# Optimization experiments

Hardware: AMD Instinct MI355X
Metric: run time of the kernel (lower is better)

## Reference

```python
import jax, jax.numpy as jnp
import numpy as np

MARGIN = 1.0


def setup_inputs() -> dict:
    key = jax.random.key(0)
    k1, k2, k3 = jax.random.split(key, 3)
    B, D, C = 16384, 256, 2000
    pred_embedding = jax.random.normal(k1, (B, D), dtype=jnp.float32)
    batch_label = jax.random.randint(k2, (B,), 0, C, dtype=jnp.int64)
    train_classes = jnp.arange(C, dtype=jnp.int64)
    train_sig = jax.random.normal(k3, (D, C), dtype=jnp.float32)
    return {
        "pred_embedding": pred_embedding,
        "batch_label": batch_label,
        "train_classes": train_classes,
        "train_sig": train_sig,
    }


def reference(pred_embedding, batch_label, train_classes, train_sig):
    # scores[j, k] = <pred_embedding[j], train_sig[:, train_classes[k]]>
    # Single GEMM replaces the per-pair dot-product loops.
    sig_cols = train_sig[:, train_classes]            # [D, C]
    scores = jnp.einsum("bd,dc->bc", pred_embedding, sig_cols)  # [B, C]
    # ground-truth class score per row: <XW_j, train_sig[:, y_j]>
    gt = jnp.einsum("bd,db->b", pred_embedding, train_sig[:, batch_label])  # [B]
    # exclude the class equal to the row label
    mask = (train_classes[None, :] != batch_label[:, None])  # [B, C] bool
    hinge = jnp.maximum(MARGIN + scores - gt[:, None], 0.0)
    loss = jnp.sum(jnp.where(mask, hinge, 0.0))
    return loss
```

## Files before the change

kernel.cpp:

```cpp
#include <hip/hip_runtime.h>

#define B_SZ 16384
#define D_SZ 256
#define C_SZ 2000
#define C_PAD 2048
#define MARGIN_F 1.0f
#define NBLK 1024

typedef float floatx16 __attribute__((ext_vector_type(16)));

__device__ inline void gld_lds16(const void* g, void* l) {
  __builtin_amdgcn_global_load_lds(
      (const __attribute__((address_space(1))) void*)g,
      (__attribute__((address_space(3))) void*)l, 16, 0, 0);
}


__device__ inline int2 pack8_fp8(const float* v) {
  int lo = __builtin_amdgcn_cvt_pk_fp8_f32(v[0], v[1], 0, false);
  lo = __builtin_amdgcn_cvt_pk_fp8_f32(v[2], v[3], lo, true);
  int hi = __builtin_amdgcn_cvt_pk_fp8_f32(v[4], v[5], 0, false);
  hi = __builtin_amdgcn_cvt_pk_fp8_f32(v[6], v[7], hi, true);
  return make_int2(lo, hi);
}
__device__ inline float rt_fp8(float x) {
  int p = __builtin_amdgcn_cvt_pk_fp8_f32(x, x, 0, false);
  return __builtin_amdgcn_cvt_f32_fp8(p, 0);
}

__global__ __launch_bounds__(256) void prep_kernel(
    const float* __restrict__ pred, const float* __restrict__ sig,
    const int* __restrict__ label, char* __restrict__ predq,
    char* __restrict__ sigq, float* __restrict__ gt) {
  int bid = (int)blockIdx.x;
  int tid = threadIdx.x;
  if (bid < 512) {
    __shared__ float ldsP[32][260];
#pragma unroll
    for (int it = 0; it < 8; it++) {
      int idx = it * 1024 + tid * 4;
      int r = idx >> 8, c = idx & 255;
      *(float4*)&ldsP[r][c] = *(const float4*)(pred + (size_t)(bid * 32 + r) * D_SZ + c);
    }
    __syncthreads();
#pragma unroll
    for (int it = 0; it < 4; it++) {
      int ch = it * 256 + tid;
      int lane = ch & 63, ks = ch >> 6;
      int r = lane & 31, kb = ks * 16 + (lane >> 5) * 8;
      float v[8];
#pragma unroll
      for (int j = 0; j < 8; j++) v[j] = ldsP[r][kb + j];
      *(int2*)(predq + ((size_t)(bid * 16 + ks) * 64 + lane) * 8) = pack8_fp8(v);
    }
    int lane = tid & 63, w = tid >> 6;
    for (int rr = 0; rr < 8; rr++) {
      int r = w * 8 + rr;
      int row = bid * 32 + r;
      int lbl = label[row];
      float s = 0.f;
#pragma unroll
      for (int i = 0; i < 4; i++)
        s += rt_fp8(ldsP[r][lane * 4 + i]) *
             rt_fp8(sig[(size_t)(lane * 4 + i) * C_SZ + lbl]);
#pragma unroll
      for (int off = 32; off > 0; off >>= 1) s += __shfl_down(s, off, 64);
      if (lane == 0) gt[row] = s;
    }
  } else {
    int ct = bid - 512;
#pragma unroll
    for (int it = 0; it < 4; it++) {
      int ch = it * 256 + tid;
      int lane = ch & 63, ks = ch >> 6;
      int col = ct * 32 + (lane & 31);
      int kb = ks * 16 + (lane >> 5) * 8;
      float v[8];
#pragma unroll
      for (int j = 0; j < 8; j++)
        v[j] = (col < C_SZ) ? sig[(size_t)(kb + j) * C_SZ + col] : 0.f;
      *(int2*)(sigq + ((size_t)(ct * 16 + ks) * 64 + lane) * 8) = pack8_fp8(v);
    }
  }
}

__global__ __launch_bounds__(256) void mfma_fused_kernel(
    const char* __restrict__ predq, const char* __restrict__ sigq,
    const float* __restrict__ gt, float* __restrict__ partial) {
  __shared__ char Bs[4096 * 8];
  __shared__ float red[4];
  int tid = threadIdx.x;
  int lane = tid & 63;
  int w = tid >> 6;
  int kh = lane >> 5, lm = lane & 31;
  int bid = (int)blockIdx.x;
  int i = bid >> 3;
  int rsb = (bid & 7) * 8 + (i & 7);
  int cg = i >> 3;

#pragma unroll
  for (int s = 0; s < 8; s++) {
    int q0 = s * 256 + w * 64;
    gld_lds16(sigq + ((size_t)cg * 2048 + q0 + lane) * 16, (void*)(Bs + (size_t)q0 * 16));
  }

  long afr[2][16];
#pragma unroll
  for (int rt = 0; rt < 2; rt++)
#pragma unroll
    for (int ks = 0; ks < 16; ks++)
      afr[rt][ks] = *(const long*)(predq +
          (((size_t)(rsb * 8 + w * 2 + rt) * 16 + ks) * 64 + lane) * 8);

  float mgv[2][16];
#pragma unroll
  for (int rt = 0; rt < 2; rt++)
#pragma unroll
    for (int reg = 0; reg < 16; reg++) {
      int row = rsb * 256 + w * 64 + rt * 32 + (reg & 3) + 8 * (reg >> 2) + 4 * kh;
      mgv[rt][reg] = MARGIN_F - gt[row];
    }
  __syncthreads();

  float sum = 0.f;
#pragma unroll
  for (int ct = 0; ct < 4; ct++) {
    floatx16 acc0 = {}, acc1 = {};
#pragma unroll
    for (int ks = 0; ks < 16; ks++) {
      long b = *(const long*)(Bs + (size_t)((ct * 16 + ks) * 64 + lane) * 8);
      acc0 = __builtin_amdgcn_mfma_f32_32x32x16_fp8_fp8(afr[0][ks], b, acc0, 0, 0, 0);
      acc1 = __builtin_amdgcn_mfma_f32_32x32x16_fp8_fp8(afr[1][ks], b, acc1, 0, 0, 0);
    }
    int col = cg * 128 + ct * 32 + lm;
    float keep = (col < C_SZ) ? 1.f : 0.f;
#pragma unroll
    for (int reg = 0; reg < 16; reg++) {
      sum += keep * fmaxf(acc0[reg] + mgv[0][reg], 0.f);
      sum += keep * fmaxf(acc1[reg] + mgv[1][reg], 0.f);
    }
  }
#pragma unroll
  for (int off = 32; off > 0; off >>= 1) sum += __shfl_down(sum, off, 64);
  if (lane == 0) red[w] = sum;
  __syncthreads();
  if (tid == 0) partial[bid] = red[0] + red[1] + red[2] + red[3];
}

__global__ __launch_bounds__(256) void reduce_kernel(
    const float* __restrict__ partial, float* __restrict__ out) {
  int tid = threadIdx.x;
  float s = 0.f;
  for (int i = tid * 4; i < NBLK; i += 1024) {
    float4 p = *(const float4*)(partial + i);
    s += p.x + p.y + p.z + p.w;
  }
#pragma unroll
  for (int off = 32; off > 0; off >>= 1) s += __shfl_down(s, off, 64);
  __shared__ float red[4];
  if ((tid & 63) == 0) red[tid >> 6] = s;
  __syncthreads();
  if (tid == 0) out[0] = red[0] + red[1] + red[2] + red[3] - (float)B_SZ * MARGIN_F;
}

extern "C" void kernel_launch(void* const* d_in, const int* in_sizes, int n_in,
                              void* d_out, int out_size, void* d_ws, size_t ws_size,
                              hipStream_t stream) {
  const float* pred  = (const float*)d_in[0];
  const int*   label = (const int*)d_in[1];
  const float* sig   = (const float*)d_in[3];
  float* out = (float*)d_out;

  float* gt      = (float*)d_ws;
  float* partial = (float*)((char*)d_ws + (64 << 10));
  char*  predq   = (char*)d_ws + (128 << 10);
  char*  sigq    = (char*)d_ws + (128 << 10) + (4 << 20);

  prep_kernel<<<576, 256, 0, stream>>>(pred, sig, label, predq, sigq, gt);
  mfma_fused_kernel<<<NBLK, 256, 0, stream>>>(predq, sigq, gt, partial);
  reduce_kernel<<<1, 256, 0, stream>>>(partial, out);
}
```

Measured before the change: 104.4 us.

## Fuse prep, GEMM-hinge and reduction into one cooperative kernel with grid syncs

Merges the three kernel launches into a single cooperative kernel of 1024 blocks. Two grid-wide barriers separate the quantization, MFMA hinge and final reduction phases, and the old three-launch path is kept as a fallback if the cooperative launch fails. The sig quantization work is spread over 256 blocks instead of 64. The goal is to remove launch gaps and tail idle time between the stages, at the cost of grid-sync overhead and a shared-memory/register budget capped to fit 4 blocks per CU so all blocks are co-resident.

```diff
diff --git a/kernel.cpp b/kernel.cpp
--- a/kernel.cpp
+++ b/kernel.cpp
@@ -1,4 +1,7 @@
 #include <hip/hip_runtime.h>
+#include <hip/hip_cooperative_groups.h>
+
+namespace cg = cooperative_groups;
 
 #define B_SZ 16384
 #define D_SZ 256
@@ -26,6 +29,126 @@
 __device__ inline float rt_fp8(float x) {
   int p = __builtin_amdgcn_cvt_pk_fp8_f32(x, x, 0, false);
   return __builtin_amdgcn_cvt_f32_fp8(p, 0);
+}
+
+__global__ __launch_bounds__(256, 4) void fused_all_kernel(
+    const float* __restrict__ pred, const float* __restrict__ sig,
+    const int* __restrict__ label, char* __restrict__ predq,
+    char* __restrict__ sigq, float* __restrict__ gt,
+    float* __restrict__ partial, float* __restrict__ out) {
+  __shared__ float ldsP[32][260];
+  __shared__ float gtS[256];
+  __shared__ float red[4];
+  char* Bs = (char*)&ldsP[0][0];
+
+  int bid = (int)blockIdx.x;
+  int tid = threadIdx.x;
+  int lane = tid & 63;
+  int w = tid >> 6;
+
+  if (bid < 512) {
+#pragma unroll
+    for (int it = 0; it < 8; it++) {
+      int idx = it * 1024 + tid * 4;
+      int r = idx >> 8, c = idx & 255;
+      *(float4*)&ldsP[r][c] = *(const float4*)(pred + (size_t)(bid * 32 + r) * D_SZ + c);
+    }
+    __syncthreads();
+#pragma unroll
+    for (int it = 0; it < 4; it++) {
+      int ch = it * 256 + tid;
+      int ln = ch & 63, ks = ch >> 6;
+      int r = ln & 31, kb = ks * 16 + (ln >> 5) * 8;
+      float v[8];
+#pragma unroll
+      for (int j = 0; j < 8; j++) v[j] = ldsP[r][kb + j];
+      *(int2*)(predq + ((size_t)(bid * 16 + ks) * 64 + ln) * 8) = pack8_fp8(v);
+    }
+    for (int rr = 0; rr < 8; rr++) {
+      int r = w * 8 + rr;
+      int row = bid * 32 + r;
+      int lbl = label[row];
+      float s = 0.f;
+#pragma unroll
+      for (int i = 0; i < 4; i++)
+        s += rt_fp8(ldsP[r][lane * 4 + i]) *
+             rt_fp8(sig[(size_t)(lane * 4 + i) * C_SZ + lbl]);
+#pragma unroll
+      for (int off = 32; off > 0; off >>= 1) s += __shfl_down(s, off, 64);
+      if (lane == 0) gt[row] = s;
+    }
+    __syncthreads();
+  } else if (bid < 768) {
+    int ch = (bid - 512) * 256 + tid;
+    int ln = ch & 63, ks = (ch >> 6) & 15, ct = ch >> 10;
+    int col = ct * 32 + (ln & 31);
+    int kb = ks * 16 + (ln >> 5) * 8;
+    float v[8];
+#pragma unroll
+    for (int j = 0; j < 8; j++)
+      v[j] = (col < C_SZ) ? sig[(size_t)(kb + j) * C_SZ + col] : 0.f;
+    *(int2*)(sigq + ((size_t)(ct * 16 + ks) * 64 + ln) * 8) = pack8_fp8(v);
+  }
+
+  cg::this_grid().sync();
+
+  int kh = lane >> 5, lm = lane & 31;
+  int i = bid >> 3;
+  int rsb = (bid & 7) * 8 + (i & 7);
+  int cg_ = i >> 3;
+
+#pragma unroll
+  for (int s = 0; s < 8; s++) {
+    int q0 = s * 256 + w * 64;
+    gld_lds16(sigq + ((size_t)cg_ * 2048 + q0 + lane) * 16, (void*)(Bs + (size_t)q0 * 16));
+  }
+  gtS[tid] = gt[rsb * 256 + tid];
+
+  long afr[2][16];
+#pragma unroll
+  for (int rt = 0; rt < 2; rt++)
+#pragma unroll
+    for (int ks = 0; ks < 16; ks++)
+      afr[rt][ks] = *(const long*)(predq +
+          (((size_t)(rsb * 8 + w * 2 + rt) * 16 + ks) * 64 + lane) * 8);
+  __syncthreads();
+
+  float sum = 0.f;
+#pragma unroll
+  for (int ct = 0; ct < 4; ct++) {
+    floatx16 acc0 = {}, acc1 = {};
+#pragma unroll
+    for (int ks = 0; ks < 16; ks++) {
+      long b = *(const long*)(Bs + (size_t)((ct * 16 + ks) * 64 + lane) * 8);
+      acc0 = __builtin_amdgcn_mfma_f32_32x32x16_fp8_fp8(afr[0][ks], b, acc0, 0, 0, 0);
+      acc1 = __builtin_amdgcn_mfma_f32_32x32x16_fp8_fp8(afr[1][ks], b, acc1, 0, 0, 0);
+    }
+    int col = cg_ * 128 + ct * 32 + lm;
+    float keep = (col < C_SZ) ? 1.f : 0.f;
+#pragma unroll
+    for (int reg = 0; reg < 16; reg++) {
+      int rl = (reg & 3) + 8 * (reg >> 2) + 4 * kh;
+      sum += keep * fmaxf(acc0[reg] + MARGIN_F - gtS[w * 64 + rl], 0.f);
+      sum += keep * fmaxf(acc1[reg] + MARGIN_F - gtS[w * 64 + 32 + rl], 0.f);
+    }
+  }
+#pragma unroll
+  for (int off = 32; off > 0; off >>= 1) sum += __shfl_down(sum, off, 64);
+  if (lane == 0) red[w] = sum;
+  __syncthreads();
+  if (tid == 0) partial[bid] = red[0] + red[1] + red[2] + red[3];
+
+  cg::this_grid().sync();
+
+  if (bid == 0) {
+    float s = 0.f;
+    for (int p = tid; p < NBLK; p += 256) s += partial[p];
+#pragma unroll
+    for (int off = 32; off > 0; off >>= 1) s += __shfl_down(s, off, 64);
+    if (lane == 0) red[w] = s;
+    __syncthreads();
+    if (tid == 0) out[0] = red[0] + red[1] + red[2] + red[3] - (float)B_SZ * MARGIN_F;
+  }
 }
 
 __global__ __launch_bounds__(256) void prep_kernel(
@@ -46,12 +169,12 @@
 #pragma unroll
     for (int it = 0; it < 4; it++) {
       int ch = it * 256 + tid;
-      int lane = ch & 63, ks = ch >> 6;
-      int r = lane & 31, kb = ks * 16 + (lane >> 5) * 8;
+      int ln = ch & 63, ks = ch >> 6;
+      int r = ln & 31, kb = ks * 16 + (ln >> 5) * 8;
       float v[8];
 #pragma unroll
       for (int j = 0; j < 8; j++) v[j] = ldsP[r][kb + j];
-      *(int2*)(predq + ((size_t)(bid * 16 + ks) * 64 + lane) * 8) = pack8_fp8(v);
+      *(int2*)(predq + ((size_t)(bid * 16 + ks) * 64 + ln) * 8) = pack8_fp8(v);
     }
     int lane = tid & 63, w = tid >> 6;
     for (int rr = 0; rr < 8; rr++) {
@@ -72,14 +195,14 @@
 #pragma unroll
     for (int it = 0; it < 4; it++) {
       int ch = it * 256 + tid;
-      int lane = ch & 63, ks = ch >> 6;
-      int col = ct * 32 + (lane & 31);
-      int kb = ks * 16 + (lane >> 5) * 8;
+      int ln = ch & 63, ks = ch >> 6;
+      int col = ct * 32 + (ln & 31);
+      int kb = ks * 16 + (ln >> 5) * 8;
       float v[8];
 #pragma unroll
       for (int j = 0; j < 8; j++)
         v[j] = (col < C_SZ) ? sig[(size_t)(kb + j) * C_SZ + col] : 0.f;
-      *(int2*)(sigq + ((size_t)(ct * 16 + ks) * 64 + lane) * 8) = pack8_fp8(v);
+      *(int2*)(sigq + ((size_t)(ct * 16 + ks) * 64 + ln) * 8) = pack8_fp8(v);
     }
   }
 }
@@ -96,14 +219,12 @@
   int bid = (int)blockIdx.x;
   int i = bid >> 3;
   int rsb = (bid & 7) * 8 + (i & 7);
-  int cg = i >> 3;
-
+  int cg_ = i >> 3;
 #pragma unroll
   for (int s = 0; s < 8; s++) {
     int q0 = s * 256 + w * 64;
-    gld_lds16(sigq + ((size_t)cg * 2048 + q0 + lane) * 16, (void*)(Bs + (size_t)q0 * 16));
-  }
-
+    gld_lds16(sigq + ((size_t)cg_ * 2048 + q0 + lane) * 16, (void*)(Bs + (size_t)q0 * 16));
+  }
   long afr[2][16];
 #pragma unroll
   for (int rt = 0; rt < 2; rt++)
@@ -111,7 +232,6 @@
     for (int ks = 0; ks < 16; ks++)
       afr[rt][ks] = *(const long*)(predq +
           (((size_t)(rsb * 8 + w * 2 + rt) * 16 + ks) * 64 + lane) * 8);
-
   float mgv[2][16];
 #pragma unroll
   for (int rt = 0; rt < 2; rt++)
@@ -121,7 +241,6 @@
       mgv[rt][reg] = MARGIN_F - gt[row];
     }
   __syncthreads();
-
   float sum = 0.f;
 #pragma unroll
   for (int ct = 0; ct < 4; ct++) {
@@ -132,7 +251,7 @@
       acc0 = __builtin_amdgcn_mfma_f32_32x32x16_fp8_fp8(afr[0][ks], b, acc0, 0, 0, 0);
       acc1 = __builtin_amdgcn_mfma_f32_32x32x16_fp8_fp8(afr[1][ks], b, acc1, 0, 0, 0);
     }
-    int col = cg * 128 + ct * 32 + lm;
+    int col = cg_ * 128 + ct * 32 + lm;
     float keep = (col < C_SZ) ? 1.f : 0.f;
 #pragma unroll
     for (int reg = 0; reg < 16; reg++) {
@@ -176,7 +295,13 @@
   char*  predq   = (char*)d_ws + (128 << 10);
   char*  sigq    = (char*)d_ws + (128 << 10) + (4 << 20);
 
-  prep_kernel<<<576, 256, 0, stream>>>(pred, sig, label, predq, sigq, gt);
-  mfma_fused_kernel<<<NBLK, 256, 0, stream>>>(predq, sigq, gt, partial);
-  reduce_kernel<<<1, 256, 0, stream>>>(partial, out);
-}
+  void* args[] = {(void*)&pred, (void*)&sig, (void*)&label, (void*)&predq,
+                  (void*)&sigq, (void*)&gt, (void*)&partial, (void*)&out};
+  hipError_t err = hipLaunchCooperativeKernel(
+      (const void*)fused_all_kernel, dim3(NBLK), dim3(256), args, 0, stream);
+  if (err != hipSuccess) {
+    prep_kernel<<<576, 256, 0, stream>>>(pred, sig, label, predq, sigq, gt);
+    mfma_fused_kernel<<<NBLK, 256, 0, stream>>>(predq, sigq, gt, partial);
+    reduce_kernel<<<1, 256, 0, stream>>>(partial, out);
+  }
+}
```

New measurement: 387.9 us. 3.72x slower.

## Split sig quantization into its own kernel, reuse it for gt, atomically reduce

Applied to the files above, without the earlier changes.

Moves the fp8 quantization of train_sig into a separate first kernel. The prep kernel then gathers each label's column from that packed buffer, with contiguous reads, instead of doing strided fp32 loads from sig to build the ground-truth score. The final reduce kernel is removed: each GEMM block atomically adds its partial, including its share of the margin correction, into an output that the first kernel zeroes. This trades one launch and scattered gathers for a new dependency between kernels and a float atomic summation order that is not deterministic.

```diff
diff --git a/kernel.cpp b/kernel.cpp
--- a/kernel.cpp
+++ b/kernel.cpp
@@ -27,66 +27,81 @@
   int p = __builtin_amdgcn_cvt_pk_fp8_f32(x, x, 0, false);
   return __builtin_amdgcn_cvt_f32_fp8(p, 0);
 }
+__device__ inline void unpack4_fp8(int w, float* o) {
+  o[0] = __builtin_amdgcn_cvt_f32_fp8(w, 0);
+  o[1] = __builtin_amdgcn_cvt_f32_fp8(w, 1);
+  o[2] = __builtin_amdgcn_cvt_f32_fp8(w, 2);
+  o[3] = __builtin_amdgcn_cvt_f32_fp8(w, 3);
+}
+
+__global__ __launch_bounds__(256) void sigq_kernel(
+    const float* __restrict__ sig, char* __restrict__ sigq,
+    float* __restrict__ out) {
+  int t = blockIdx.x * 256 + threadIdx.x;
+  if (t == 0) out[0] = 0.f;
+  int ln = t & 63, ks = (t >> 6) & 15, ct = t >> 10;
+  int col = ct * 32 + (ln & 31);
+  int kb = ks * 16 + (ln >> 5) * 8;
+  float v[8];
+#pragma unroll
+  for (int j = 0; j < 8; j++)
+    v[j] = (col < C_SZ) ? sig[(size_t)(kb + j) * C_SZ + col] : 0.f;
+  *(int2*)(sigq + (size_t)t * 8) = pack8_fp8(v);
+}
 
 __global__ __launch_bounds__(256) void prep_kernel(
-    const float* __restrict__ pred, const float* __restrict__ sig,
+    const float* __restrict__ pred, const char* __restrict__ sigq,
     const int* __restrict__ label, char* __restrict__ predq,
-    char* __restrict__ sigq, float* __restrict__ gt) {
+    float* __restrict__ gt) {
+  __shared__ float ldsP[32][260];
   int bid = (int)blockIdx.x;
   int tid = threadIdx.x;
-  if (bid < 512) {
-    __shared__ float ldsP[32][260];
+  int lane = tid & 63;
+  int w = tid >> 6;
 #pragma unroll
-    for (int it = 0; it < 8; it++) {
-      int idx = it * 1024 + tid * 4;
-      int r = idx >> 8, c = idx & 255;
-      *(float4*)&ldsP[r][c] = *(const float4*)(pred + (size_t)(bid * 32 + r) * D_SZ + c);
-    }
-    __syncthreads();
+  for (int it = 0; it < 8; it++) {
+    int idx = it * 1024 + tid * 4;
+    int r = idx >> 8, c = idx & 255;
+    *(float4*)&ldsP[r][c] = *(const float4*)(pred + (size_t)(bid * 32 + r) * D_SZ + c);
+  }
+  __syncthreads();
 #pragma unroll
-    for (int it = 0; it < 4; it++) {
-      int ch = it * 256 + tid;
-      int lane = ch & 63, ks = ch >> 6;
-      int r = lane & 31, kb = ks * 16 + (lane >> 5) * 8;
-      float v[8];
+  for (int it = 0; it < 4; it++) {
+    int ch = it * 256 + tid;
+    int ln = ch & 63, ks = ch >> 6;
+    int r = ln & 31, kb = ks * 16 + (ln >> 5) * 8;
+    float v[8];
 #pragma unroll
-      for (int j = 0; j < 8; j++) v[j] = ldsP[r][kb + j];
-      *(int2*)(predq + ((size_t)(bid * 16 + ks) * 64 + lane) * 8) = pack8_fp8(v);
-    }
-    int lane = tid & 63, w = tid >> 6;
-    for (int rr = 0; rr < 8; rr++) {
-      int r = w * 8 + rr;
-      int row = bid * 32 + r;
-      int lbl = label[row];
-      float s = 0.f;
+    for (int j = 0; j < 8; j++) v[j] = ldsP[r][kb + j];
+    *(int2*)(predq + ((size_t)(bid * 16 + ks) * 64 + ln) * 8) = pack8_fp8(v);
+  }
+  int l = lane & 31;
+  int half = lane >> 5;
 #pragma unroll
-      for (int i = 0; i < 4; i++)
-        s += rt_fp8(ldsP[r][lane * 4 + i]) *
-             rt_fp8(sig[(size_t)(lane * 4 + i) * C_SZ + lbl]);
+  for (int it = 0; it < 4; it++) {
+    int r = w * 8 + it * 2 + half;
+    int row = bid * 32 + r;
+    int lbl = label[row];
+    int tile = lbl >> 5, l5 = lbl & 31;
+    int ks = l >> 1, kh = l & 1;
+    int2 p8 = *(const int2*)(sigq +
+        (((size_t)(tile * 16 + ks) * 64) + kh * 32 + l5) * 8);
+    float sv[8];
+    unpack4_fp8(p8.x, sv);
+    unpack4_fp8(p8.y, sv + 4);
+    float s = 0.f;
 #pragma unroll
-      for (int off = 32; off > 0; off >>= 1) s += __shfl_down(s, off, 64);
-      if (lane == 0) gt[row] = s;
-    }
-  } else {
-    int ct = bid - 512;
+    for (int j = 0; j < 8; j++)
+      s += rt_fp8(ldsP[r][l * 8 + j]) * sv[j];
 #pragma unroll
-    for (int it = 0; it < 4; it++) {
-      int ch = it * 256 + tid;
-      int lane = ch & 63, ks = ch >> 6;
-      int col = ct * 32 + (lane & 31);
-      int kb = ks * 16 + (lane >> 5) * 8;
-      float v[8];
-#pragma unroll
-      for (int j = 0; j < 8; j++)
-        v[j] = (col < C_SZ) ? sig[(size_t)(kb + j) * C_SZ + col] : 0.f;
-      *(int2*)(sigq + ((size_t)(ct * 16 + ks) * 64 + lane) * 8) = pack8_fp8(v);
-    }
+    for (int off = 16; off > 0; off >>= 1) s += __shfl_down(s, off, 32);
+    if (l == 0) gt[row] = s;
   }
 }
 
 __global__ __launch_bounds__(256) void mfma_fused_kernel(
     const char* __restrict__ predq, const char* __restrict__ sigq,
-    const float* __restrict__ gt, float* __restrict__ partial) {
+    const float* __restrict__ gt, float* __restrict__ out) {
   __shared__ char Bs[4096 * 8];
   __shared__ float red[4];
   int tid = threadIdx.x;
@@ -144,23 +159,9 @@
   for (int off = 32; off > 0; off >>= 1) sum += __shfl_down(sum, off, 64);
   if (lane == 0) red[w] = sum;
   __syncthreads();
-  if (tid == 0) partial[bid] = red[0] + red[1] + red[2] + red[3];
-}
-
-__global__ __launch_bounds__(256) void reduce_kernel(
-    const float* __restrict__ partial, float* __restrict__ out) {
-  int tid = threadIdx.x;
-  float s = 0.f;
-  for (int i = tid * 4; i < NBLK; i += 1024) {
-    float4 p = *(const float4*)(partial + i);
-    s += p.x + p.y + p.z + p.w;
-  }
-#pragma unroll
-  for (int off = 32; off > 0; off >>= 1) s += __shfl_down(s, off, 64);
-  __shared__ float red[4];
-  if ((tid & 63) == 0) red[tid >> 6] = s;
-  __syncthreads();
-  if (tid == 0) out[0] = red[0] + red[1] + red[2] + red[3] - (float)B_SZ * MARGIN_F;
+  if (tid == 0)
+    atomicAdd(out, red[0] + red[1] + red[2] + red[3]
+                   - (float)B_SZ * MARGIN_F / (float)NBLK);
 }
 
 extern "C" void kernel_launch(void* const* d_in, const int* in_sizes, int n_in,
@@ -171,12 +172,11 @@
   const float* sig   = (const float*)d_in[3];
   float* out = (float*)d_out;
 
-  float* gt      = (float*)d_ws;
-  float* partial = (float*)((char*)d_ws + (64 << 10));
-  char*  predq   = (char*)d_ws + (128 << 10);
-  char*  sigq    = (char*)d_ws + (128 << 10) + (4 << 20);
+  float* gt    = (float*)d_ws;
+  char*  predq = (char*)d_ws + (128 << 10);
+  char*  sigq  = (char*)d_ws + (128 << 10) + (4 << 20);
 
-  prep_kernel<<<576, 256, 0, stream>>>(pred, sig, label, predq, sigq, gt);
-  mfma_fused_kernel<<<NBLK, 256, 0, stream>>>(predq, sigq, gt, partial);
-  reduce_kernel<<<1, 256, 0, stream>>>(partial, out);
+  sigq_kernel<<<256, 256, 0, stream>>>(sig, sigq, out);
+  prep_kernel<<<512, 256, 0, stream>>>(pred, sigq, label, predq, gt);
+  mfma_fused_kernel<<<NBLK, 256, 0, stream>>>(predq, sigq, gt, out);
 }
```

Result: faster. 97.95 us (-6.1%).
